# Optimization experiments

Hardware: AMD Instinct MI355X
Metric: run time of the kernel (lower is better)

The kernel has to match this reference:

```python
import jax, jax.numpy as jnp
import numpy as np

CHANNELS = 256
C_QK = CHANNELS // 8


def setup_inputs() -> dict:
    key = jax.random.key(0)
    ks = jax.random.split(key, 7)
    b, c, h, w = 8, CHANNELS, 64, 64
    x = jax.random.normal(ks[0], (b, c, h, w), dtype=jnp.float32)
    # 1x1 conv weights stored as [out_ch, in_ch]; biases [out_ch]
    s = 1.0 / np.sqrt(c)
    wq = jax.random.uniform(ks[1], (C_QK, c), jnp.float32, -s, s)
    bq = jax.random.uniform(ks[2], (C_QK,), jnp.float32, -s, s)
    wk = jax.random.uniform(ks[3], (C_QK, c), jnp.float32, -s, s)
    bk = jax.random.uniform(ks[4], (C_QK,), jnp.float32, -s, s)
    wv = jax.random.uniform(ks[5], (c, c), jnp.float32, -s, s)
    bv = jax.random.uniform(ks[6], (c,), jnp.float32, -s, s)
    return {"x": x, "wq": wq, "bq": bq, "wk": wk, "bk": bk, "wv": wv, "bv": bv}


def reference(x, wq, bq, wk, bk, wv, bv):
    b, c, h, w = x.shape
    xf = x.reshape(b, c, h * w)  # [b, c, n]
    # 1x1 convs == per-pixel linear projections
    q = jnp.einsum('oc,bcn->bon', wq, xf) + bq[None, :, None]  # [b, c//8, n]
    k = jnp.einsum('oc,bcn->bon', wk, xf) + bk[None, :, None]  # [b, c//8, n]
    v = jnp.einsum('oc,bcn->bon', wv, xf) + bv[None, :, None]  # [b, c, n]
    # attention[i, j] = q_i . k_j  (no scaling, matching the torch code)
    attn = jnp.einsum('bdi,bdj->bij', q, k)  # [b, n, n]
    attn = jax.nn.softmax(attn, axis=-1)
    # out[:, :, i] = sum_j attn[i, j] * v[:, :, j]
    out = jnp.einsum('bij,bcj->bci', attn, v)  # [b, c, n]
    return out.reshape(b, c, h, w)
```

## Files before the change

kernel.cpp:

```cpp
#include <hip/hip_runtime.h>
#include <stdint.h>

#define NB 8
#define NC 256
#define ND 32
#define NN 4096
#define QT 64
#define KT 32
#define NBUF 4

typedef __attribute__((ext_vector_type(8))) short short8;
typedef __attribute__((ext_vector_type(4))) float float4_;

#define MFMA16(a,b,c) __builtin_amdgcn_mfma_f32_16x16x32_bf16((a),(b),(c),0,0,0)

#if __has_builtin(__builtin_amdgcn_exp2f)
#define EXP2(x) __builtin_amdgcn_exp2f(x)
#else
#define EXP2(x) exp2f(x)
#endif
#define L2E 1.44269504088896f
#define SCB (24.0f * L2E)

__device__ __forceinline__ uint16_t f2bf(float f) {
  uint32_t u = __builtin_bit_cast(uint32_t, f);
  u += 0x7fffu + ((u >> 16) & 1u);
  return (uint16_t)(u >> 16);
}
__device__ __forceinline__ float bf2f(uint16_t h) {
  uint32_t u = (uint32_t)h << 16;
  return __builtin_bit_cast(float, u);
}
__device__ __forceinline__ short8 ld8(const uint16_t* p) {
  return *reinterpret_cast<const short8*>(p);
}
__device__ __forceinline__ uint32_t cvtpk(float lo, float hi) {
  uint32_t r;
  asm("v_cvt_pk_bf16_f32 %0, %1, %2" : "=v"(r) : "v"(lo), "v"(hi));
  return r;
}
__device__ __forceinline__ void async16(const uint16_t* g, uint16_t* l) {
  __builtin_amdgcn_global_load_lds(
      (const __attribute__((address_space(1))) uint32_t*)g,
      (__attribute__((address_space(3))) uint32_t*)l, 16, 0, 0);
}
__device__ __forceinline__ void fbar() {
  asm volatile("" ::: "memory");
  __builtin_amdgcn_s_barrier();
  asm volatile("" ::: "memory");
}

__global__ __launch_bounds__(256) void k_prep(
    const float* __restrict__ x, const float* __restrict__ wq,
    const float* __restrict__ wk, const float* __restrict__ wv,
    uint16_t* __restrict__ xTh, uint16_t* __restrict__ xTl,
    uint16_t* __restrict__ Wh, uint16_t* __restrict__ Wl, int use_xl)
{
  int bx = blockIdx.x, tid = threadIdx.x;
  if (bx >= 2048) {
    int e = (bx - 2048) * 256 + tid;
    int r = e >> 8;
    float w = (r < 32) ? wq[e] : (r < 64) ? wk[e - 32 * 256] : wv[e - 64 * 256];
    uint16_t h = f2bf(w);
    Wh[e] = h;
    Wl[e] = f2bf(w - bf2f(h));
    return;
  }
  __shared__ uint32_t tile[64][65];
  int b = bx >> 8, t = bx & 255;
  int c0 = (t >> 6) << 6, n0 = (t & 63) << 6;
  const float* xb = x + ((size_t)b * NC + c0) * NN + n0;
  int cc = tid >> 4, nw = (tid & 15) << 2;
  for (int i = 0; i < 4; i++) {
    int c = cc + 16 * i;
    float4_ v = *reinterpret_cast<const float4_*>(xb + (size_t)c * NN + nw);
    for (int u = 0; u < 4; u++) {
      uint16_t h = f2bf(v[u]);
      uint16_t l = f2bf(v[u] - bf2f(h));
      tile[c][nw + u] = (uint32_t)h | ((uint32_t)l << 16);
    }
  }
  __syncthreads();
  int cw = (tid & 15) << 2, nn = tid >> 4;
  for (int i = 0; i < 4; i++) {
    int n = nn + 16 * i;
    uint32_t p0 = tile[cw + 0][n], p1 = tile[cw + 1][n];
    uint32_t p2 = tile[cw + 2][n], p3 = tile[cw + 3][n];
    size_t o = ((size_t)b * NN + n0 + n) * NC + c0 + cw;
    *(uint32_t*)(xTh + o)     = (p0 & 0xffffu) | (p1 << 16);
    *(uint32_t*)(xTh + o + 2) = (p2 & 0xffffu) | (p3 << 16);
    if (use_xl) {
      *(uint32_t*)(xTl + o)     = (p0 >> 16) | (p1 & 0xffff0000u);
      *(uint32_t*)(xTl + o + 2) = (p2 >> 16) | (p3 & 0xffff0000u);
    }
  }
}

__global__ __launch_bounds__(256) void k_qkv(
    const uint16_t* __restrict__ xTh, const uint16_t* __restrict__ xTl,
    const uint16_t* __restrict__ Wh, const uint16_t* __restrict__ Wl,
    const float* __restrict__ bq, const float* __restrict__ bk,
    const float* __restrict__ bv,
    uint16_t* __restrict__ Qh, uint16_t* __restrict__ Ql,
    uint16_t* __restrict__ Kh, uint16_t* __restrict__ Kl,
    uint16_t* __restrict__ V, int use_xl, int use_lo)
{
  int b = blockIdx.x & 7, n0 = (blockIdx.x >> 3) * 64;
  int tid = threadIdx.x, wid = tid >> 6, lane = tid & 63;
  int l15 = lane & 15, quad = lane >> 4;
  int nb = n0 + wid * 16;
  float4_ acc[20];
  for (int m = 0; m < 20; m++) acc[m] = (float4_){0.f, 0.f, 0.f, 0.f};
  for (int ks = 0; ks < 8; ks++) {
    size_t xa = ((size_t)b * NN + nb + l15) * NC + ks * 32 + quad * 8;
    short8 bh = ld8(xTh + xa);
    short8 blo;
    if (use_xl) blo = ld8(xTl + xa);
    for (int mt = 0; mt < 20; mt++) {
      size_t wa = (size_t)(16 * mt + l15) * NC + ks * 32 + quad * 8;
      short8 ah = ld8(Wh + wa);
      acc[mt] = MFMA16(ah, bh, acc[mt]);
      if (mt < 4) {
        short8 al = ld8(Wl + wa);
        acc[mt] = MFMA16(al, bh, acc[mt]);
      }
      if (use_xl) acc[mt] = MFMA16(ah, blo, acc[mt]);
    }
  }
  int n = nb + l15;
  for (int mt = 0; mt < 20; mt++) {
    for (int r = 0; r < 4; r++) {
      int row = 16 * mt + quad * 4 + r;
      float v = acc[mt][r];
      if (mt < 2) {
        v = (v + bq[row]) * L2E;
        size_t o = ((size_t)b * NN + n) * ND + row;
        uint16_t h = f2bf(v);
        Qh[o] = h;
        if (use_lo) Ql[o] = f2bf(v - bf2f(h));
      } else if (mt < 4) {
        int rk = row - 32;
        v += bk[rk];
        size_t o = ((size_t)b * NN + n) * ND + rk;
        uint16_t h = f2bf(v);
        Kh[o] = h;
        if (use_lo) Kl[o] = f2bf(v - bf2f(h));
      } else {
        int c = row - 64;
        v += bv[c];
        V[((size_t)b * NC + c) * NN + n] = f2bf(v);
      }
    }
  }
}

__global__ __launch_bounds__(512, 4) void k_attn(
    const uint16_t* __restrict__ Qh, const uint16_t* __restrict__ Ql,
    const uint16_t* __restrict__ Kh, const uint16_t* __restrict__ Kl,
    const uint16_t* __restrict__ V, float* __restrict__ out, int use_lo)
{
  __shared__ uint16_t sV[NBUF][256][KT];
  __shared__ uint16_t sP[2][4][16][40];
  __shared__ float sL[QT];

  int bx = blockIdx.x;
  int b = bx & 7;
  int q0 = (bx >> 3) * QT;
  int tid = threadIdx.x, wid = tid >> 6, lane = tid & 63;
  int l15 = lane & 15, quad = lane >> 4;
  const size_t qkb = (size_t)b * NN * ND;
  const uint16_t* Vb = V + (size_t)b * NC * NN;
  const bool heavy = (wid < 4);

  int sw = (l15 >> 1) & 3;

  const uint16_t* gp0; const uint16_t* gp1;
  const uint16_t* gp2; const uint16_t* gp3;
  uint32_t off0, off1, off2, off3;
  if (!heavy) {
#define INITGP(i, GP, OFF)                                   \
    { int sl = (wid - 4) * 256 + 64 * i + lane;              \
      int c = sl >> 2;                                       \
      int q2s = (sl & 3) ^ ((sl >> 3) & 3);                  \
      GP = Vb + (size_t)c * NN + q2s * 8;                    \
      OFF = (uint32_t)(((wid - 4) * 4 + i) * 512); }
    INITGP(0, gp0, off0) INITGP(1, gp1, off1)
    INITGP(2, gp2, off2) INITGP(3, gp3, off3)
#undef INITGP
  }
  auto stage = [&](int s) {
    uint16_t* base = &sV[0][0][0] + (size_t)(s & 3) * 8192;
    async16(gp0, base + off0); gp0 += KT;
    async16(gp1, base + off1); gp1 += KT;
    async16(gp2, base + off2); gp2 += KT;
    async16(gp3, base + off3); gp3 += KT;
  };

  float4_ acc[2][4];
  for (int m = 0; m < 2; m++) for (int n = 0; n < 4; n++)
    acc[m][n] = (float4_){0.f, 0.f, 0.f, 0.f};
  float l_part = 0.f;

  short8 qfh, qfl, kh0, kh1, kl0, kl1;
  const uint16_t* pKh = Kh + qkb + (size_t)l15 * ND + quad * 8;
  const uint16_t* pKl = Kl + qkb + (size_t)l15 * ND + quad * 8;

  auto qkt = [&](int sb, short8 h0, short8 h1, short8 lo0, short8 lo1) {
    float4_ S0 = (float4_){0.f, 0.f, 0.f, 0.f}, S1 = S0;
    S0 = MFMA16(h0, qfh, S0);
    S1 = MFMA16(h1, qfh, S1);
    if (use_lo) {
      S0 = MFMA16(lo0, qfh, S0); S0 = MFMA16(h0, qfl, S0);
      S1 = MFMA16(lo1, qfh, S1); S1 = MFMA16(h1, qfl, S1);
    }
    float p0[4], p1[4];
#pragma unroll
    for (int r = 0; r < 4; r++) {
      p0[r] = EXP2(S0[r] - SCB);
      p1[r] = EXP2(S1[r] - SCB);
    }
    l_part += ((p0[0] + p0[1]) + (p0[2] + p0[3])) +
              ((p1[0] + p1[1]) + (p1[2] + p1[3]));
    uint2 w0, w1;
    w0.x = cvtpk(p0[0], p0[1]); w0.y = cvtpk(p0[2], p0[3]);
    w1.x = cvtpk(p1[0], p1[1]); w1.y = cvtpk(p1[2], p1[3]);
    *reinterpret_cast<uint2*>(&sP[sb][wid][l15][4 * quad]) = w0;
    *reinterpret_cast<uint2*>(&sP[sb][wid][l15][16 + 4 * quad]) = w1;
  };

  if (heavy) {
    size_t a = qkb + (size_t)(q0 + wid * 16 + l15) * ND + quad * 8;
    qfh = ld8(Qh + a);
    if (use_lo) qfl = ld8(Ql + a);
    short8 t0 = ld8(pKh), t1 = ld8(pKh + 512), tl0, tl1;
    if (use_lo) { tl0 = ld8(pKl); tl1 = ld8(pKl + 512); }
    qkt(0, t0, t1, tl0, tl1);
    kh0 = ld8(pKh + 1024); kh1 = ld8(pKh + 1536);
    if (use_lo) { kl0 = ld8(pKl + 1024); kl1 = ld8(pKl + 1536); }
    pKh += 2048; pKl += 2048;
    asm volatile("s_waitcnt lgkmcnt(0)" ::: "memory");
  } else {
    stage(0); stage(1); stage(2);
    asm volatile("s_waitcnt vmcnt(8)" ::: "memory");
  }
  fbar();

  for (int j = 0; j < NN / KT; j++) {
    int buf = j & 3;
    int pb = j & 1;
    if (heavy) {
      short8 nh0, nh1, nl0, nl1;
      if (j < NN / KT - 2) {
        nh0 = ld8(pKh); nh1 = ld8(pKh + 512);
        if (use_lo) { nl0 = ld8(pKl); nl1 = ld8(pKl + 512); }
        pKh += 1024; pKl += 1024;
      }
      if (j < NN / KT - 1)
        qkt(pb ^ 1, kh0, kh1, kl0, kl1);
      kh0 = nh0; kh1 = nh1;
      if (use_lo) { kl0 = nl0; kl1 = nl1; }
    } else {
      if (j < NN / KT - 3) stage(j + 3);
    }
    short8 bfP[4];
#pragma unroll
    for (int qt = 0; qt < 4; qt++)
      bfP[qt] = ld8(&sP[pb][qt][l15][quad * 8]);
#pragma unroll
    for (int mt = 0; mt < 2; mt++) {
      short8 af = ld8(&sV[buf][wid * 32 + 16 * mt + l15][(quad ^ sw) * 8]);
#pragma unroll
      for (int qt = 0; qt < 4; qt++)
        acc[mt][qt] = MFMA16(af, bfP[qt], acc[mt][qt]);
    }
    if (!heavy) {
      if (j < NN / KT - 3)
        asm volatile("s_waitcnt vmcnt(8)" ::: "memory");
      else
        asm volatile("s_waitcnt vmcnt(0)" ::: "memory");
    }
    asm volatile("s_waitcnt lgkmcnt(0)" ::: "memory");
    fbar();
  }

  if (heavy) {
    float l_tot = l_part;
    l_tot += __shfl_xor(l_tot, 16);
    l_tot += __shfl_xor(l_tot, 32);
    if (quad == 0) sL[wid * 16 + l15] = l_tot;
  }
  __syncthreads();
  float linv[4];
  for (int qt = 0; qt < 4; qt++) linv[qt] = 1.0f / sL[qt * 16 + l15];
  for (int mt = 0; mt < 2; mt++)
    for (int qt = 0; qt < 4; qt++)
      for (int r = 0; r < 4; r++) {
        int c = wid * 32 + 16 * mt + quad * 4 + r;
        int q = q0 + qt * 16 + l15;
        out[((size_t)(b * NC + c)) * NN + q] = acc[mt][qt][r] * linv[qt];
      }
}

extern "C" void kernel_launch(void* const* d_in, const int* in_sizes, int n_in,
                              void* d_out, int out_size, void* d_ws, size_t ws_size,
                              hipStream_t stream)
{
  const float* x  = (const float*)d_in[0];
  const float* wq = (const float*)d_in[1];
  const float* bq = (const float*)d_in[2];
  const float* wk = (const float*)d_in[3];
  const float* bk = (const float*)d_in[4];
  const float* wv = (const float*)d_in[5];
  const float* bv = (const float*)d_in[6];
  float* out = (float*)d_out;

  const size_t szXT = (size_t)NB * NN * NC * 2;
  const size_t szW  = (size_t)320 * 256 * 2;
  const size_t szQK = (size_t)NB * NN * ND * 2;
  const size_t szV  = (size_t)NB * NC * NN * 2;
  size_t needA = 2 * szXT + 2 * szW + 4 * szQK + szV;
  size_t needB = szXT + 2 * szW + 4 * szQK + szV;
  int use_xl = ws_size >= needA;
  int use_lo = ws_size >= needB;

  char* p = (char*)d_ws;
  uint16_t* xTh = (uint16_t*)p; p += szXT;
  uint16_t* xTl = use_xl ? (uint16_t*)p : xTh; if (use_xl) p += szXT;
  uint16_t* Wh = (uint16_t*)p; p += szW;
  uint16_t* Wl = (uint16_t*)p; p += szW;
  uint16_t* Qh = (uint16_t*)p; p += szQK;
  uint16_t* Ql = use_lo ? (uint16_t*)p : xTh; if (use_lo) p += szQK;
  uint16_t* Kh = (uint16_t*)p; p += szQK;
  uint16_t* Kl = use_lo ? (uint16_t*)p : xTh; if (use_lo) p += szQK;
  uint16_t* Vw = (uint16_t*)p;

  hipLaunchKernelGGL(k_prep, dim3(2368), dim3(256), 0, stream,
                     x, wq, wk, wv, xTh, xTl, Wh, Wl, use_xl);
  hipLaunchKernelGGL(k_qkv, dim3(512), dim3(256), 0, stream,
                     xTh, xTl, Wh, Wl, bq, bk, bv, Qh, Ql, Kh, Kl, Vw,
                     use_xl, use_lo);
  hipLaunchKernelGGL(k_attn, dim3(512), dim3(512), 0, stream,
                     Qh, Ql, Kh, Kl, Vw, out, use_lo);
}
```

Measured before the change: 277.7 us.

## Drop warp specialization; all waves compute QK and read V directly from global

Replaces the split where four waves computed QK^T/softmax and four waves staged V into LDS via async global-to-LDS loads. Now all eight waves each compute a 16x32 slice of the score tile over a 64-key step, and each wave loads its V fragments straight from global memory into registers. This removes the V LDS buffers and their async pipeline, and row sums are combined across two waves at the end. It risks exposed global-load latency on V, since nothing prefetches it ahead of the MFMAs, and it doubles the per-step key tile.

```diff
diff --git a/kernel.cpp b/kernel.cpp
--- a/kernel.cpp
+++ b/kernel.cpp
@@ -6,8 +6,7 @@
 #define ND 32
 #define NN 4096
 #define QT 64
-#define KT 32
-#define NBUF 4
+#define KTI 64
 
 typedef __attribute__((ext_vector_type(8))) short short8;
 typedef __attribute__((ext_vector_type(4))) float float4_;
@@ -38,11 +37,6 @@
   uint32_t r;
   asm("v_cvt_pk_bf16_f32 %0, %1, %2" : "=v"(r) : "v"(lo), "v"(hi));
   return r;
-}
-__device__ __forceinline__ void async16(const uint16_t* g, uint16_t* l) {
-  __builtin_amdgcn_global_load_lds(
-      (const __attribute__((address_space(1))) uint32_t*)g,
-      (__attribute__((address_space(3))) uint32_t*)l, 16, 0, 0);
 }
 __device__ __forceinline__ void fbar() {
   asm volatile("" ::: "memory");
@@ -159,9 +153,8 @@
     const uint16_t* __restrict__ Kh, const uint16_t* __restrict__ Kl,
     const uint16_t* __restrict__ V, float* __restrict__ out, int use_lo)
 {
-  __shared__ uint16_t sV[NBUF][256][KT];
-  __shared__ uint16_t sP[2][4][16][40];
-  __shared__ float sL[QT];
+  __shared__ uint16_t sP[2][64][72];
+  __shared__ float sL[2][QT];
 
   int bx = blockIdx.x;
   int b = bx & 7;
@@ -170,40 +163,20 @@
   int l15 = lane & 15, quad = lane >> 4;
   const size_t qkb = (size_t)b * NN * ND;
   const uint16_t* Vb = V + (size_t)b * NC * NN;
-  const bool heavy = (wid < 4);
-
-  int sw = (l15 >> 1) & 3;
-
-  const uint16_t* gp0; const uint16_t* gp1;
-  const uint16_t* gp2; const uint16_t* gp3;
-  uint32_t off0, off1, off2, off3;
-  if (!heavy) {
-#define INITGP(i, GP, OFF)                                   \
-    { int sl = (wid - 4) * 256 + 64 * i + lane;              \
-      int c = sl >> 2;                                       \
-      int q2s = (sl & 3) ^ ((sl >> 3) & 3);                  \
-      GP = Vb + (size_t)c * NN + q2s * 8;                    \
-      OFF = (uint32_t)(((wid - 4) * 4 + i) * 512); }
-    INITGP(0, gp0, off0) INITGP(1, gp1, off1)
-    INITGP(2, gp2, off2) INITGP(3, gp3, off3)
-#undef INITGP
-  }
-  auto stage = [&](int s) {
-    uint16_t* base = &sV[0][0][0] + (size_t)(s & 3) * 8192;
-    async16(gp0, base + off0); gp0 += KT;
-    async16(gp1, base + off1); gp1 += KT;
-    async16(gp2, base + off2); gp2 += KT;
-    async16(gp3, base + off3); gp3 += KT;
-  };
+  const int qtw = wid >> 1;
+  const int ktb = (wid & 1) * 2;
+
+  size_t qa = qkb + (size_t)(q0 + qtw * 16 + l15) * ND + quad * 8;
+  short8 qfh = ld8(Qh + qa), qfl;
+  if (use_lo) qfl = ld8(Ql + qa);
+
+  const uint16_t* pKh = Kh + qkb + (size_t)(ktb * 16 + l15) * ND + quad * 8;
+  const uint16_t* pKl = Kl + qkb + (size_t)(ktb * 16 + l15) * ND + quad * 8;
 
   float4_ acc[2][4];
   for (int m = 0; m < 2; m++) for (int n = 0; n < 4; n++)
     acc[m][n] = (float4_){0.f, 0.f, 0.f, 0.f};
   float l_part = 0.f;
-
-  short8 qfh, qfl, kh0, kh1, kl0, kl1;
-  const uint16_t* pKh = Kh + qkb + (size_t)l15 * ND + quad * 8;
-  const uint16_t* pKl = Kl + qkb + (size_t)l15 * ND + quad * 8;
 
   auto qkt = [&](int sb, short8 h0, short8 h1, short8 lo0, short8 lo1) {
     float4_ S0 = (float4_){0.f, 0.f, 0.f, 0.f}, S1 = S0;
@@ -224,76 +197,68 @@
     uint2 w0, w1;
     w0.x = cvtpk(p0[0], p0[1]); w0.y = cvtpk(p0[2], p0[3]);
     w1.x = cvtpk(p1[0], p1[1]); w1.y = cvtpk(p1[2], p1[3]);
-    *reinterpret_cast<uint2*>(&sP[sb][wid][l15][4 * quad]) = w0;
-    *reinterpret_cast<uint2*>(&sP[sb][wid][l15][16 + 4 * quad]) = w1;
+    uint16_t* row = &sP[sb][qtw * 16 + l15][0];
+    *reinterpret_cast<uint2*>(row + ktb * 16 + 4 * quad) = w0;
+    *reinterpret_cast<uint2*>(row + ktb * 16 + 16 + 4 * quad) = w1;
   };
 
-  if (heavy) {
-    size_t a = qkb + (size_t)(q0 + wid * 16 + l15) * ND + quad * 8;
-    qfh = ld8(Qh + a);
-    if (use_lo) qfl = ld8(Ql + a);
-    short8 t0 = ld8(pKh), t1 = ld8(pKh + 512), tl0, tl1;
-    if (use_lo) { tl0 = ld8(pKl); tl1 = ld8(pKl + 512); }
-    qkt(0, t0, t1, tl0, tl1);
-    kh0 = ld8(pKh + 1024); kh1 = ld8(pKh + 1536);
-    if (use_lo) { kl0 = ld8(pKl + 1024); kl1 = ld8(pKl + 1536); }
-    pKh += 2048; pKl += 2048;
-    asm volatile("s_waitcnt lgkmcnt(0)" ::: "memory");
-  } else {
-    stage(0); stage(1); stage(2);
-    asm volatile("s_waitcnt vmcnt(8)" ::: "memory");
-  }
+  {
+    short8 h0 = ld8(pKh), h1 = ld8(pKh + 512), lo0, lo1;
+    if (use_lo) { lo0 = ld8(pKl); lo1 = ld8(pKl + 512); }
+    pKh += KTI * ND; pKl += KTI * ND;
+    qkt(0, h0, h1, lo0, lo1);
+  }
+  asm volatile("s_waitcnt lgkmcnt(0)" ::: "memory");
   fbar();
 
-  for (int j = 0; j < NN / KT; j++) {
-    int buf = j & 3;
+  const uint16_t* vp = Vb + (size_t)(wid * 32 + l15) * NN + quad * 8;
+
+  for (int j = 0; j < NN / KTI; j++) {
     int pb = j & 1;
-    if (heavy) {
-      short8 nh0, nh1, nl0, nl1;
-      if (j < NN / KT - 2) {
-        nh0 = ld8(pKh); nh1 = ld8(pKh + 512);
-        if (use_lo) { nl0 = ld8(pKl); nl1 = ld8(pKl + 512); }
-        pKh += 1024; pKl += 1024;
-      }
-      if (j < NN / KT - 1)
-        qkt(pb ^ 1, kh0, kh1, kl0, kl1);
-      kh0 = nh0; kh1 = nh1;
-      if (use_lo) { kl0 = nl0; kl1 = nl1; }
-    } else {
-      if (j < NN / KT - 3) stage(j + 3);
-    }
-    short8 bfP[4];
-#pragma unroll
-    for (int qt = 0; qt < 4; qt++)
-      bfP[qt] = ld8(&sP[pb][qt][l15][quad * 8]);
-#pragma unroll
-    for (int mt = 0; mt < 2; mt++) {
-      short8 af = ld8(&sV[buf][wid * 32 + 16 * mt + l15][(quad ^ sw) * 8]);
-#pragma unroll
-      for (int qt = 0; qt < 4; qt++)
-        acc[mt][qt] = MFMA16(af, bfP[qt], acc[mt][qt]);
-    }
-    if (!heavy) {
-      if (j < NN / KT - 3)
-        asm volatile("s_waitcnt vmcnt(8)" ::: "memory");
-      else
-        asm volatile("s_waitcnt vmcnt(0)" ::: "memory");
-    }
+    short8 nh0, nh1, nl0, nl1;
+    if (j < NN / KTI - 1) {
+      nh0 = ld8(pKh); nh1 = ld8(pKh + 512);
+      if (use_lo) { nl0 = ld8(pKl); nl1 = ld8(pKl + 512); }
+      pKh += KTI * ND; pKl += KTI * ND;
+    }
+#pragma unroll
+    for (int kh = 0; kh < 2; kh++) {
+      short8 af0 = ld8(vp + kh * 32);
+      short8 af1 = ld8(vp + 16 * NN + kh * 32);
+      short8 bp0 = ld8(&sP[pb][ 0 + l15][kh * 32 + quad * 8]);
+      short8 bp1 = ld8(&sP[pb][16 + l15][kh * 32 + quad * 8]);
+      short8 bp2 = ld8(&sP[pb][32 + l15][kh * 32 + quad * 8]);
+      short8 bp3 = ld8(&sP[pb][48 + l15][kh * 32 + quad * 8]);
+      acc[0][0] = MFMA16(af0, bp0, acc[0][0]);
+      acc[0][1] = MFMA16(af0, bp1, acc[0][1]);
+      acc[0][2] = MFMA16(af0, bp2, acc[0][2]);
+      acc[0][3] = MFMA16(af0, bp3, acc[0][3]);
+      acc[1][0] = MFMA16(af1, bp0, acc[1][0]);
+      acc[1][1] = MFMA16(af1, bp1, acc[1][1]);
+      acc[1][2] = MFMA16(af1, bp2, acc[1][2]);
+      acc[1][3] = MFMA16(af1, bp3, acc[1][3]);
+    }
+    vp += KTI;
+    if (j < NN / KTI - 1)
+      qkt(pb ^ 1, nh0, nh1, nl0, nl1);
     asm volatile("s_waitcnt lgkmcnt(0)" ::: "memory");
     fbar();
   }
 
-  if (heavy) {
-    float l_tot = l_part;
-    l_tot += __shfl_xor(l_tot, 16);
-    l_tot += __shfl_xor(l_tot, 32);
-    if (quad == 0) sL[wid * 16 + l15] = l_tot;
-  }
+  float l_tot = l_part;
+  l_tot += __shfl_xor(l_tot, 16);
+  l_tot += __shfl_xor(l_tot, 32);
+  if (quad == 0) sL[wid & 1][qtw * 16 + l15] = l_tot;
   __syncthreads();
   float linv[4];
-  for (int qt = 0; qt < 4; qt++) linv[qt] = 1.0f / sL[qt * 16 + l15];
+#pragma unroll
+  for (int qt = 0; qt < 4; qt++)
+    linv[qt] = 1.0f / (sL[0][qt * 16 + l15] + sL[1][qt * 16 + l15]);
+#pragma unroll
   for (int mt = 0; mt < 2; mt++)
+#pragma unroll
     for (int qt = 0; qt < 4; qt++)
+#pragma unroll
       for (int r = 0; r < 4; r++) {
         int c = wid * 32 + 16 * mt + quad * 4 + r;
         int q = q0 + qt * 16 + l15;
```

After: 331.9 us. 1.19x slower.

## Stage packed QKV weights through double-buffered LDS with async loads

Applied to the files above, without the earlier changes.

The prep kernel now stores the bf16 hi/lo weights in a per-k-slice padded layout (40-element row stride), keeping lo parts only for the Q/K rows. The QKV projection kernel loads each slice into a double-buffered shared-memory tile with global_load_lds and prefetches the next x fragment. This replaces repeated per-wave global weight loads with shared LDS reads and overlaps the fetches with MFMA work. It adds about 60KB of LDS per block, which may lower occupancy, plus a barrier per k-step.

```diff
diff --git a/kernel.cpp b/kernel.cpp
--- a/kernel.cpp
+++ b/kernel.cpp
@@ -54,16 +54,19 @@
     const float* __restrict__ x, const float* __restrict__ wq,
     const float* __restrict__ wk, const float* __restrict__ wv,
     uint16_t* __restrict__ xTh, uint16_t* __restrict__ xTl,
-    uint16_t* __restrict__ Wh, uint16_t* __restrict__ Wl, int use_xl)
+    uint16_t* __restrict__ WhP, uint16_t* __restrict__ WlP, int use_xl)
 {
   int bx = blockIdx.x, tid = threadIdx.x;
   if (bx >= 2048) {
     int e = (bx - 2048) * 256 + tid;
-    int r = e >> 8;
-    float w = (r < 32) ? wq[e] : (r < 64) ? wk[e - 32 * 256] : wv[e - 64 * 256];
+    int row = e >> 8, col = e & 255;
+    float w = (row < 32) ? wq[e] : (row < 64) ? wk[e - 32 * 256]
+                                              : wv[e - 64 * 256];
     uint16_t h = f2bf(w);
-    Wh[e] = h;
-    Wl[e] = f2bf(w - bf2f(h));
+    int ks = col >> 5, c5 = col & 31;
+    WhP[(size_t)ks * 12800 + row * 40 + c5] = h;
+    if (row < 64)
+      WlP[(size_t)ks * 2560 + row * 40 + c5] = f2bf(w - bf2f(h));
     return;
   }
   __shared__ uint32_t tile[64][65];
@@ -98,35 +101,70 @@
 
 __global__ __launch_bounds__(256) void k_qkv(
     const uint16_t* __restrict__ xTh, const uint16_t* __restrict__ xTl,
-    const uint16_t* __restrict__ Wh, const uint16_t* __restrict__ Wl,
+    const uint16_t* __restrict__ WhP, const uint16_t* __restrict__ WlP,
     const float* __restrict__ bq, const float* __restrict__ bk,
     const float* __restrict__ bv,
     uint16_t* __restrict__ Qh, uint16_t* __restrict__ Ql,
     uint16_t* __restrict__ Kh, uint16_t* __restrict__ Kl,
     uint16_t* __restrict__ V, int use_xl, int use_lo)
 {
+  __shared__ uint16_t sW[2][15360];
+
   int b = blockIdx.x & 7, n0 = (blockIdx.x >> 3) * 64;
   int tid = threadIdx.x, wid = tid >> 6, lane = tid & 63;
   int l15 = lane & 15, quad = lane >> 4;
   int nb = n0 + wid * 16;
+
+  auto stageW = [&](int ks, int buf) {
+    const uint16_t* srcH = WhP + (size_t)ks * 12800;
+    const uint16_t* srcL = WlP + (size_t)ks * 2560;
+    uint16_t* dst = &sW[buf][0];
+#pragma unroll
+    for (int i = 0; i < 8; i++) {
+      int idx = i * 256 + tid;
+      if (idx < 1920) {
+        const uint16_t* g = (idx < 1600) ? (srcH + (size_t)idx * 8)
+                                         : (srcL + (size_t)(idx - 1600) * 8);
+        async16(g, dst + (size_t)idx * 8);
+      }
+    }
+  };
+
   float4_ acc[20];
   for (int m = 0; m < 20; m++) acc[m] = (float4_){0.f, 0.f, 0.f, 0.f};
+
+  size_t xa0 = ((size_t)b * NN + nb + l15) * NC + quad * 8;
+  short8 bh = ld8(xTh + xa0), blo;
+  if (use_xl) blo = ld8(xTl + xa0);
+
+  stageW(0, 0);
+  __syncthreads();
+
   for (int ks = 0; ks < 8; ks++) {
-    size_t xa = ((size_t)b * NN + nb + l15) * NC + ks * 32 + quad * 8;
-    short8 bh = ld8(xTh + xa);
-    short8 blo;
-    if (use_xl) blo = ld8(xTl + xa);
+    int buf = ks & 1;
+    if (ks < 7) stageW(ks + 1, buf ^ 1);
+    short8 nbh, nblo;
+    if (ks < 7) {
+      size_t xn = xa0 + (size_t)(ks + 1) * 32;
+      nbh = ld8(xTh + xn);
+      if (use_xl) nblo = ld8(xTl + xn);
+    }
+    const uint16_t* wb = &sW[buf][0];
+#pragma unroll
     for (int mt = 0; mt < 20; mt++) {
-      size_t wa = (size_t)(16 * mt + l15) * NC + ks * 32 + quad * 8;
-      short8 ah = ld8(Wh + wa);
+      short8 ah = ld8(wb + (16 * mt + l15) * 40 + quad * 8);
       acc[mt] = MFMA16(ah, bh, acc[mt]);
       if (mt < 4) {
-        short8 al = ld8(Wl + wa);
+        short8 al = ld8(wb + 12800 + (16 * mt + l15) * 40 + quad * 8);
         acc[mt] = MFMA16(al, bh, acc[mt]);
       }
       if (use_xl) acc[mt] = MFMA16(ah, blo, acc[mt]);
     }
-  }
+    __syncthreads();
+    bh = nbh;
+    if (use_xl) blo = nblo;
+  }
+
   int n = nb + l15;
   for (int mt = 0; mt < 20; mt++) {
     for (int r = 0; r < 4; r++) {
@@ -315,19 +353,20 @@
   float* out = (float*)d_out;
 
   const size_t szXT = (size_t)NB * NN * NC * 2;
-  const size_t szW  = (size_t)320 * 256 * 2;
+  const size_t szWh = (size_t)8 * 320 * 40 * 2;
+  const size_t szWl = (size_t)8 * 64 * 40 * 2;
   const size_t szQK = (size_t)NB * NN * ND * 2;
   const size_t szV  = (size_t)NB * NC * NN * 2;
-  size_t needA = 2 * szXT + 2 * szW + 4 * szQK + szV;
-  size_t needB = szXT + 2 * szW + 4 * szQK + szV;
+  size_t needA = 2 * szXT + szWh + szWl + 4 * szQK + szV;
+  size_t needB = szXT + szWh + szWl + 4 * szQK + szV;
   int use_xl = ws_size >= needA;
   int use_lo = ws_size >= needB;
 
   char* p = (char*)d_ws;
   uint16_t* xTh = (uint16_t*)p; p += szXT;
   uint16_t* xTl = use_xl ? (uint16_t*)p : xTh; if (use_xl) p += szXT;
-  uint16_t* Wh = (uint16_t*)p; p += szW;
-  uint16_t* Wl = (uint16_t*)p; p += szW;
+  uint16_t* WhP = (uint16_t*)p; p += szWh;
+  uint16_t* WlP = (uint16_t*)p; p += szWl;
   uint16_t* Qh = (uint16_t*)p; p += szQK;
   uint16_t* Ql = use_lo ? (uint16_t*)p : xTh; if (use_lo) p += szQK;
   uint16_t* Kh = (uint16_t*)p; p += szQK;
@@ -335,9 +374,9 @@
   uint16_t* Vw = (uint16_t*)p;
 
   hipLaunchKernelGGL(k_prep, dim3(2368), dim3(256), 0, stream,
-                     x, wq, wk, wv, xTh, xTl, Wh, Wl, use_xl);
+                     x, wq, wk, wv, xTh, xTl, WhP, WlP, use_xl);
   hipLaunchKernelGGL(k_qkv, dim3(512), dim3(256), 0, stream,
-                     xTh, xTl, Wh, Wl, bq, bk, bv, Qh, Ql, Kh, Kl, Vw,
+                     xTh, xTl, WhP, WlP, bq, bk, bv, Qh, Ql, Kh, Kl, Vw,
                      use_xl, use_lo);
   hipLaunchKernelGGL(k_attn, dim3(512), dim3(512), 0, stream,
                      Qh, Ql, Kh, Kl, Vw, out, use_lo);
```

After: 246.6 us. 1.13x faster.
